# Optimization experiments

Measured on AMD Instinct MI355X. Metric: run time of the kernel, lower is better.

Reference implementation:

```python
import jax, jax.numpy as jnp
import numpy as np

TOPK = 2


def setup_inputs() -> dict:
    key = jax.random.key(0)
    k1, k2 = jax.random.split(key)
    B, N, D, E, C = 4, 2048, 2048, 8, 512
    token_inputs = jax.random.normal(k1, (B, N, D), dtype=jnp.float32)
    # bottleneck_in.weight.t() stacked over experts: [E, D, C]; scaled like a real init
    bottleneck_weights = jax.random.normal(k2, (E, D, C), dtype=jnp.float32) * 0.02
    return {
        "token_inputs": token_inputs,
        "bottleneck_weights": bottleneck_weights,
        "expert_capacity": 640,
    }


def _routing(router_probs, expert_capacity, topk):
    # router_probs: [B, N, E]
    B, N, E = router_probs.shape
    _, expert_indices = jax.lax.top_k(router_probs, topk)      # [B, N, topk]
    idx = jnp.transpose(expert_indices, (0, 2, 1)).reshape(B, topk * N)
    expert_mask = jax.nn.one_hot(idx, E, dtype=jnp.int32)       # [B, topk*N, E]
    token_priority = jnp.cumsum(expert_mask, axis=1) * expert_mask - 1
    token_priority = token_priority.reshape(B, topk, N, E)
    token_priority = jnp.transpose(token_priority, (0, 2, 1, 3))  # [B, N, topk, E]
    token_priority = jnp.max(token_priority, axis=2)              # [B, N, E]
    # one-hot over capacity; negative (-1) and >= capacity priorities map to all-zero rows
    cap_range = jnp.arange(expert_capacity, dtype=jnp.int32)
    dispatch = (token_priority[..., None] == cap_range).astype(jnp.float32)  # [B,N,E,C]
    combine = router_probs[..., None] * dispatch                            # [B,N,E,C]
    return dispatch, combine


def reference(token_inputs, bottleneck_weights, expert_capacity):
    # activation_cache: [B, N, E, Cb]
    activation_cache = jnp.einsum("bnd,edc->bnec", token_inputs, bottleneck_weights)
    router_logits = jnp.sqrt(jnp.sum(activation_cache * activation_cache, axis=-1))  # [B,N,E]
    router_probs = jax.nn.softmax(router_logits, axis=-1)
    dispatch, combine = _routing(router_probs, expert_capacity, TOPK)
    return jnp.stack([dispatch, combine], axis=0)  # [2, B, N, E, capacity]
```

## Files before the change

kernel.cpp:

```cpp
#include <hip/hip_runtime.h>
#include <math.h>

constexpr int Bb = 4, Nn = 2048, Dd = 2048, Ee = 8, Cbn = 512;
constexpr int Mm = Bb * Nn;

typedef _Float16 half8 __attribute__((ext_vector_type(8)));
typedef float floatx16 __attribute__((ext_vector_type(16)));

#define GLL16(g, l)                                                     \
  __builtin_amdgcn_global_load_lds(                                     \
      (const __attribute__((address_space(1))) void*)(g),               \
      (__attribute__((address_space(3))) void*)(l), 16, 0, 0)

#define MFMA_F16(a, b, c) __builtin_amdgcn_mfma_f32_32x32x16_f16(a, b, c, 0, 0, 0)


__global__ __launch_bounds__(256) void transpose_w(const float* __restrict__ W,
                                                   _Float16* __restrict__ WT) {
  const int kt = blockIdx.x;
  const int ct = blockIdx.y;
  const int e = blockIdx.z;
  __shared__ _Float16 thi[64][72];
  __shared__ _Float16 tlo[64][72];
  const int tx = threadIdx.x & 15, ty = threadIdx.x >> 4;
  const float* src = W + ((size_t)(e * 2048 + kt * 64)) * 512 + ct * 64;
#pragma unroll
  for (int p = 0; p < 4; ++p) {
    int kk = ty + p * 16;
    float4 v = *(const float4*)(src + (size_t)kk * 512 + tx * 4);
    _Float16 hh;
    hh = (_Float16)v.x; thi[tx * 4 + 0][kk] = hh; tlo[tx * 4 + 0][kk] = (_Float16)(v.x - (float)hh);
    hh = (_Float16)v.y; thi[tx * 4 + 1][kk] = hh; tlo[tx * 4 + 1][kk] = (_Float16)(v.y - (float)hh);
    hh = (_Float16)v.z; thi[tx * 4 + 2][kk] = hh; tlo[tx * 4 + 2][kk] = (_Float16)(v.z - (float)hh);
    hh = (_Float16)v.w; thi[tx * 4 + 3][kk] = hh; tlo[tx * 4 + 3][kk] = (_Float16)(v.w - (float)hh);
  }
  __syncthreads();
  const int ntile = e * 4 + (ct >> 1);
#pragma unroll
  for (int p = 0; p < 2; ++p) {
    int unit = threadIdx.x + p * 256;
    int ch = unit >> 6;
    int cc = unit & 63;
    int ktile = kt * 2 + (ch >> 2);
    int chunk = ch & 3;
    int row = (ct & 1) * 64 + cc;
    _Float16* dst = WT + ((size_t)(ntile * 64 + ktile)) * 8192 + chunk * 1024 + row * 8;
    *(half8*)dst = *(const half8*)(&thi[cc][ch * 8]);
    *(half8*)(dst + 4096) = *(const half8*)(&tlo[cc][ch * 8]);
  }
}

__global__ __launch_bounds__(256) void split_x(const float* __restrict__ X,
                                               _Float16* __restrict__ XT) {
  const int mt = blockIdx.x;
  const int kt = blockIdx.y;
  const int tid = threadIdx.x;
  _Float16* tb = XT + ((size_t)(mt * 64 + kt)) * 8192;
#pragma unroll
  for (int p = 0; p < 2; ++p) {
    const int u = tid + p * 256;
    const int chunk = u & 3;
    const int row = u >> 2;
    const float* src = X + ((size_t)(mt * 128 + row)) * 2048 + kt * 32 + chunk * 8;
    float4 a = *(const float4*)src;
    float4 b = *(const float4*)(src + 4);
    float f[8] = {a.x, a.y, a.z, a.w, b.x, b.y, b.z, b.w};
    half8 hi, lo;
#pragma unroll
    for (int j = 0; j < 8; ++j) {
      _Float16 hh = (_Float16)f[j];
      hi[j] = hh;
      lo[j] = (_Float16)(f[j] - (float)hh);
    }
    *(half8*)(tb + chunk * 1024 + row * 8) = hi;
    *(half8*)(tb + 4096 + chunk * 1024 + row * 8) = lo;
  }
}

__global__ __launch_bounds__(256) void gemm_mfma(const _Float16* __restrict__ XT,
                                                 const _Float16* __restrict__ WT,
                                                 float* __restrict__ partial) {
  const int bid = blockIdx.x;
  const int st = bid >> 8;
  const int stm = st & 3;
  const int stn = st >> 2;
  const int li = bid & 255;
  const int mtile = stm * 16 + (li >> 4);
  const int ntile = stn * 16 + (li & 15);

  const int tid = threadIdx.x;
  const int wave = tid >> 6, lane = tid & 63;
  const int wm = wave >> 1, wn = wave & 1;
  const int h = lane >> 5;

  __shared__ __align__(16) char lds[65536];

  const char* aSrc = (const char*)XT + (size_t)mtile * 64 * 16384 + wave * 4096 + lane * 16;
  const char* bSrc = (const char*)WT + (size_t)ntile * 64 * 16384 + wave * 4096 + lane * 16;

  const int rowA0 = wm * 64 + (lane & 31);
  const int rB0 = wn * 64 + (lane & 31);

  int aOff[2][2], bOff[2][2];
#pragma unroll
  for (int s = 0; s < 2; ++s)
#pragma unroll
    for (int hl = 0; hl < 2; ++hl) {
      aOff[s][hl] = hl * 8192 + (s * 2 + h) * 2048 + rowA0 * 16;
      bOff[s][hl] = 16384 + hl * 8192 + (s * 2 + h) * 2048 + rB0 * 16;
    }

  floatx16 acc00 = {}, acc01 = {}, acc10 = {}, acc11 = {};

#pragma unroll
  for (int q = 0; q < 4; ++q) {
    GLL16(aSrc + q * 1024, lds + wave * 4096 + q * 1024);
    GLL16(bSrc + q * 1024, lds + 16384 + wave * 4096 + q * 1024);
  }
  __syncthreads();

  for (int kt = 0; kt < 64; ++kt) {
    const int cur = kt & 1;
    if (kt < 63) {
      const char* a = aSrc + (size_t)(kt + 1) * 16384;
      const char* b = bSrc + (size_t)(kt + 1) * 16384;
      char* base = lds + (cur ^ 1) * 32768 + wave * 4096;
#pragma unroll
      for (int q = 0; q < 4; ++q) {
        GLL16(a + q * 1024, base + q * 1024);
        GLL16(b + q * 1024, base + 16384 + q * 1024);
      }
    }
    const char* L = lds + cur * 32768;
#pragma unroll
    for (int s = 0; s < 2; ++s) {
      half8 ah0 = *(const half8*)(L + aOff[s][0]);
      half8 ah1 = *(const half8*)(L + aOff[s][0] + 512);
      half8 al0 = *(const half8*)(L + aOff[s][1]);
      half8 al1 = *(const half8*)(L + aOff[s][1] + 512);
      half8 bh0 = *(const half8*)(L + bOff[s][0]);
      half8 bh1 = *(const half8*)(L + bOff[s][0] + 512);
      half8 bl0 = *(const half8*)(L + bOff[s][1]);
      half8 bl1 = *(const half8*)(L + bOff[s][1] + 512);
      acc00 = MFMA_F16(ah0, bh0, acc00);
      acc00 = MFMA_F16(ah0, bl0, acc00);
      acc00 = MFMA_F16(al0, bh0, acc00);
      acc01 = MFMA_F16(ah0, bh1, acc01);
      acc01 = MFMA_F16(ah0, bl1, acc01);
      acc01 = MFMA_F16(al0, bh1, acc01);
      acc10 = MFMA_F16(ah1, bh0, acc10);
      acc10 = MFMA_F16(ah1, bl0, acc10);
      acc10 = MFMA_F16(al1, bh0, acc10);
      acc11 = MFMA_F16(ah1, bh1, acc11);
      acc11 = MFMA_F16(ah1, bl1, acc11);
      acc11 = MFMA_F16(al1, bh1, acc11);
    }
    __syncthreads();
  }

  float myv = 0.f;
#pragma unroll
  for (int i = 0; i < 2; ++i) {
    const floatx16& c0 = i ? acc10 : acc00;
    const floatx16& c1 = i ? acc11 : acc01;
#pragma unroll
    for (int reg = 0; reg < 16; ++reg) {
      float v = c0[reg] * c0[reg] + c1[reg] * c1[reg];
#pragma unroll
      for (int m = 1; m <= 16; m <<= 1) v += __shfl_xor(v, m, 64);
      if ((lane & 31) == i * 16 + reg) myv = v;
    }
  }
  {
    const int i = (lane & 31) >> 4;
    const int reg = lane & 15;
    const int row = i * 32 + (reg & 3) + 8 * (reg >> 2) + 4 * h;
    const int token = mtile * 128 + wm * 64 + row;
    const int slice = ntile * 2 + wn;
    partial[(size_t)token * 64 + slice] = myv;
  }
}

__global__ void route_kernel(const float* __restrict__ partial,
                             int* __restrict__ idx1, int* __restrict__ idx2,
                             float* __restrict__ p1, float* __restrict__ p2) {
  int t = blockIdx.x * blockDim.x + threadIdx.x;
  if (t >= Mm) return;
  float l[Ee];
  float mx = -1e30f;
#pragma unroll
  for (int e = 0; e < Ee; ++e) {
    float s = 0.f;
#pragma unroll
    for (int u = 0; u < 8; ++u) s += partial[(size_t)t * 64 + e * 8 + u];
    l[e] = sqrtf(s);
    mx = fmaxf(mx, l[e]);
  }
  float p[Ee];
  float s = 0.f;
#pragma unroll
  for (int e = 0; e < Ee; ++e) {
    p[e] = expf(l[e] - mx);
    s += p[e];
  }
  float inv = 1.f / s;
  int i1 = 0;
  float b1 = l[0];
#pragma unroll
  for (int e = 1; e < Ee; ++e)
    if (l[e] > b1) { b1 = l[e]; i1 = e; }
  int i2 = -1;
  float b2 = -1e30f;
#pragma unroll
  for (int e = 0; e < Ee; ++e)
    if (e != i1 && l[e] > b2) { b2 = l[e]; i2 = e; }
  idx1[t] = i1;
  idx2[t] = i2;
  p1[t] = p[i1] * inv;
  p2[t] = p[i2] * inv;
}

__global__ void scan_kernel(const int* __restrict__ idx1,
                            const int* __restrict__ idx2,
                            int* __restrict__ prios) {
  const int b = blockIdx.x;
  const int tid = threadIdx.x;
  __shared__ int cnts[256][8];
  int cnt[8] = {0, 0, 0, 0, 0, 0, 0, 0};
  int eloc[16];
  const int base_p = tid * 16;
#pragma unroll
  for (int i = 0; i < 16; ++i) {
    int p = base_p + i;
    int k = p >> 11;
    int n = p & (Nn - 1);
    int e = (k == 0 ? idx1 : idx2)[b * Nn + n];
    eloc[i] = e;
    cnt[e]++;
  }
#pragma unroll
  for (int e = 0; e < 8; ++e) cnts[tid][e] = cnt[e];
  __syncthreads();
  if (tid < 8) {
    int run = 0;
    for (int i = 0; i < 256; ++i) {
      int v = cnts[i][tid];
      cnts[i][tid] = run;
      run += v;
    }
  }
  __syncthreads();
  int base[8];
#pragma unroll
  for (int e = 0; e < 8; ++e) base[e] = cnts[tid][e];
#pragma unroll
  for (int i = 0; i < 16; ++i) {
    int e = eloc[i];
    prios[b * 2 * Nn + base_p + i] = base[e]++;
  }
}

__global__ __launch_bounds__(256) void zscatter_kernel(const int* __restrict__ idx1,
                                                       const int* __restrict__ idx2,
                                                       const float* __restrict__ p1,
                                                       const float* __restrict__ p2,
                                                       const int* __restrict__ prios,
                                                       float* __restrict__ out, int cap) {
  const int t = blockIdx.x;
  const int ec = Ee * cap;
  float4* o1 = (float4*)(out + (size_t)t * ec);
  float4* o2 = (float4*)(out + (size_t)(Mm + t) * ec);
  const float4 z = make_float4(0.f, 0.f, 0.f, 0.f);
  const int n4 = ec / 4;
  for (int i = threadIdx.x; i < n4; i += 256) {
    o1[i] = z;
    o2[i] = z;
  }
  __syncthreads();
  if (threadIdx.x == 0) {
    const int b = t >> 11;
    const int n = t & (Nn - 1);
    int e = idx1[t];
    int p = prios[b * 2 * Nn + n];
    if (p < cap) {
      out[(size_t)t * ec + e * cap + p] = 1.f;
      out[(size_t)(Mm + t) * ec + e * cap + p] = p1[t];
    }
    e = idx2[t];
    p = prios[b * 2 * Nn + Nn + n];
    if (p < cap) {
      out[(size_t)t * ec + e * cap + p] = 1.f;
      out[(size_t)(Mm + t) * ec + e * cap + p] = p2[t];
    }
  }
}

extern "C" void kernel_launch(void* const* d_in, const int* in_sizes, int n_in,
                              void* d_out, int out_size, void* d_ws, size_t ws_size,
                              hipStream_t stream) {
  const float* X = (const float*)d_in[0];
  const float* W = (const float*)d_in[1];
  float* out = (float*)d_out;
  const int cap = out_size / (2 * Bb * Nn * Ee);

  char* ws = (char*)d_ws;
  _Float16* WT = (_Float16*)ws;
  float* partial = (float*)(ws + 33554432ull);
  int* idx1 = (int*)(ws + 35651584ull);
  int* idx2 = idx1 + Mm;
  float* p1 = (float*)(idx2 + Mm);
  float* p2 = p1 + Mm;
  int* prios = (int*)(p2 + Mm);

  _Float16* XT = (_Float16*)d_out;

  transpose_w<<<dim3(32, 8, 8), 256, 0, stream>>>(W, WT);
  split_x<<<dim3(64, 64), 256, 0, stream>>>(X, XT);
  gemm_mfma<<<2048, 256, 0, stream>>>(XT, WT, partial);
  route_kernel<<<Mm / 256, 256, 0, stream>>>(partial, idx1, idx2, p1, p2);
  scan_kernel<<<Bb, 256, 0, stream>>>(idx1, idx2, prios);
  zscatter_kernel<<<Mm, 256, 0, stream>>>(idx1, idx2, p1, p2, prios, out, cap);
}
```

Measured before the change: 777.3 us.

## Enlarge GEMM tiles to 256x256 with 4-stage LDS pipeline and K16 layout

```diff
diff --git a/kernel.cpp b/kernel.cpp
--- a/kernel.cpp
+++ b/kernel.cpp
@@ -35,33 +35,32 @@
     hh = (_Float16)v.w; thi[tx * 4 + 3][kk] = hh; tlo[tx * 4 + 3][kk] = (_Float16)(v.w - (float)hh);
   }
   __syncthreads();
-  const int ntile = e * 4 + (ct >> 1);
+  const int nt = e * 4 + (ct >> 1);
 #pragma unroll
   for (int p = 0; p < 2; ++p) {
     int unit = threadIdx.x + p * 256;
     int ch = unit >> 6;
     int cc = unit & 63;
-    int ktile = kt * 2 + (ch >> 2);
-    int chunk = ch & 3;
+    int kt16 = kt * 4 + (ch >> 1);
+    int chunk = ch & 1;
     int row = (ct & 1) * 64 + cc;
-    _Float16* dst = WT + ((size_t)(ntile * 64 + ktile)) * 8192 + chunk * 1024 + row * 8;
+    _Float16* dst = WT + ((size_t)(nt * 128 + kt16)) * 4096 + chunk * 1024 + row * 8;
     *(half8*)dst = *(const half8*)(&thi[cc][ch * 8]);
-    *(half8*)(dst + 4096) = *(const half8*)(&tlo[cc][ch * 8]);
+    *(half8*)(dst + 2048) = *(const half8*)(&tlo[cc][ch * 8]);
   }
 }
 
 __global__ __launch_bounds__(256) void split_x(const float* __restrict__ X,
                                                _Float16* __restrict__ XT) {
   const int mt = blockIdx.x;
-  const int kt = blockIdx.y;
+  const int kb = blockIdx.y;
   const int tid = threadIdx.x;
-  _Float16* tb = XT + ((size_t)(mt * 64 + kt)) * 8192;
 #pragma unroll
   for (int p = 0; p < 2; ++p) {
     const int u = tid + p * 256;
-    const int chunk = u & 3;
+    const int c4 = u & 3;
     const int row = u >> 2;
-    const float* src = X + ((size_t)(mt * 128 + row)) * 2048 + kt * 32 + chunk * 8;
+    const float* src = X + ((size_t)(mt * 128 + row)) * 2048 + kb * 32 + c4 * 8;
     float4 a = *(const float4*)src;
     float4 b = *(const float4*)(src + 4);
     float f[8] = {a.x, a.y, a.z, a.w, b.x, b.y, b.z, b.w};
@@ -72,112 +71,138 @@
       hi[j] = hh;
       lo[j] = (_Float16)(f[j] - (float)hh);
     }
-    *(half8*)(tb + chunk * 1024 + row * 8) = hi;
-    *(half8*)(tb + 4096 + chunk * 1024 + row * 8) = lo;
-  }
-}
-
-__global__ __launch_bounds__(256) void gemm_mfma(const _Float16* __restrict__ XT,
+    const int kt16 = kb * 2 + (c4 >> 1);
+    const int chunk = c4 & 1;
+    _Float16* dst = XT + ((size_t)(mt * 128 + kt16)) * 4096 + chunk * 1024 + row * 8;
+    *(half8*)dst = hi;
+    *(half8*)(dst + 2048) = lo;
+  }
+}
+
+__global__ __launch_bounds__(512) void gemm_mfma(const _Float16* __restrict__ XT,
                                                  const _Float16* __restrict__ WT,
                                                  float* __restrict__ partial) {
   const int bid = blockIdx.x;
-  const int st = bid >> 8;
-  const int stm = st & 3;
-  const int stn = st >> 2;
-  const int li = bid & 255;
-  const int mtile = stm * 16 + (li >> 4);
-  const int ntile = stn * 16 + (li & 15);
+  const int swz = (bid & 7) * 64 + (bid >> 3);
+  const int bM = swz >> 4;
+  const int bN = swz & 15;
 
   const int tid = threadIdx.x;
-  const int wave = tid >> 6, lane = tid & 63;
-  const int wm = wave >> 1, wn = wave & 1;
-  const int h = lane >> 5;
-
-  __shared__ __align__(16) char lds[65536];
-
-  const char* aSrc = (const char*)XT + (size_t)mtile * 64 * 16384 + wave * 4096 + lane * 16;
-  const char* bSrc = (const char*)WT + (size_t)ntile * 64 * 16384 + wave * 4096 + lane * 16;
-
-  const int rowA0 = wm * 64 + (lane & 31);
-  const int rB0 = wn * 64 + (lane & 31);
-
-  int aOff[2][2], bOff[2][2];
-#pragma unroll
-  for (int s = 0; s < 2; ++s)
-#pragma unroll
-    for (int hl = 0; hl < 2; ++hl) {
-      aOff[s][hl] = hl * 8192 + (s * 2 + h) * 2048 + rowA0 * 16;
-      bOff[s][hl] = 16384 + hl * 8192 + (s * 2 + h) * 2048 + rB0 * 16;
-    }
-
-  floatx16 acc00 = {}, acc01 = {}, acc10 = {}, acc11 = {};
-
-#pragma unroll
-  for (int q = 0; q < 4; ++q) {
-    GLL16(aSrc + q * 1024, lds + wave * 4096 + q * 1024);
-    GLL16(bSrc + q * 1024, lds + 16384 + wave * 4096 + q * 1024);
-  }
-  __syncthreads();
-
-  for (int kt = 0; kt < 64; ++kt) {
-    const int cur = kt & 1;
-    if (kt < 63) {
-      const char* a = aSrc + (size_t)(kt + 1) * 16384;
-      const char* b = bSrc + (size_t)(kt + 1) * 16384;
-      char* base = lds + (cur ^ 1) * 32768 + wave * 4096;
-#pragma unroll
-      for (int q = 0; q < 4; ++q) {
-        GLL16(a + q * 1024, base + q * 1024);
-        GLL16(b + q * 1024, base + 16384 + q * 1024);
+  const int w = tid >> 6, l = tid & 63;
+  const int wm = w >> 2, wn = w & 3;
+  const int h = l >> 5, l31 = l & 31;
+
+  __shared__ __align__(16) char lds[131072];
+
+  const char* XTb = (const char*)XT;
+  const char* WTb = (const char*)WT;
+  const char* srcA[2];
+  const char* srcB[2];
+  int ldsAo[2], ldsBo[2];
+#pragma unroll
+  for (int q = 0; q < 2; ++q) {
+    const int i3 = q * 4 + (w >> 1);
+    srcA[q] = XTb + ((size_t)((bM * 2 + (i3 >> 2)) * 128)) * 8192 +
+              (i3 & 3) * 2048 + (w & 1) * 1024 + l * 16;
+    srcB[q] = WTb + ((size_t)((bN * 2 + (i3 >> 2)) * 128)) * 8192 +
+              (i3 & 3) * 2048 + (w & 1) * 1024 + l * 16;
+    ldsAo[q] = q * 8192 + w * 1024;
+    ldsBo[q] = 16384 + q * 8192 + w * 1024;
+  }
+
+  int aoff[4][2], boff[2][2];
+#pragma unroll
+  for (int mf = 0; mf < 4; ++mf)
+#pragma unroll
+    for (int hl = 0; hl < 2; ++hl)
+      aoff[mf][hl] = wm * 8192 + hl * 4096 + h * 2048 + (mf * 32 + l31) * 16;
+#pragma unroll
+  for (int nf = 0; nf < 2; ++nf)
+#pragma unroll
+    for (int hl = 0; hl < 2; ++hl)
+      boff[nf][hl] = 16384 + (wn >> 1) * 8192 + hl * 4096 + h * 2048 +
+                     ((wn & 1) * 64 + nf * 32 + l31) * 16;
+
+  floatx16 acc[4][2] = {};
+
+  auto stage = [&](int t) {
+    const size_t ko = (size_t)t * 8192;
+    char* base = lds + (t & 3) * 32768;
+#pragma unroll
+    for (int q = 0; q < 2; ++q) {
+      GLL16(srcA[q] + ko, base + ldsAo[q]);
+      GLL16(srcB[q] + ko, base + ldsBo[q]);
+    }
+  };
+  auto compute = [&](int t) {
+    const char* Lb = lds + (t & 3) * 32768;
+    half8 ah[4], al[4], bh[2], bl[2];
+#pragma unroll
+    for (int mf = 0; mf < 4; ++mf) {
+      ah[mf] = *(const half8*)(Lb + aoff[mf][0]);
+      al[mf] = *(const half8*)(Lb + aoff[mf][1]);
+    }
+#pragma unroll
+    for (int nf = 0; nf < 2; ++nf) {
+      bh[nf] = *(const half8*)(Lb + boff[nf][0]);
+      bl[nf] = *(const half8*)(Lb + boff[nf][1]);
+    }
+    __builtin_amdgcn_s_setprio(1);
+#pragma unroll
+    for (int mf = 0; mf < 4; ++mf)
+#pragma unroll
+      for (int nf = 0; nf < 2; ++nf) {
+        acc[mf][nf] = MFMA_F16(ah[mf], bh[nf], acc[mf][nf]);
+        acc[mf][nf] = MFMA_F16(ah[mf], bl[nf], acc[mf][nf]);
+        acc[mf][nf] = MFMA_F16(al[mf], bh[nf], acc[mf][nf]);
       }
-    }
-    const char* L = lds + cur * 32768;
-#pragma unroll
-    for (int s = 0; s < 2; ++s) {
-      half8 ah0 = *(const half8*)(L + aOff[s][0]);
-      half8 ah1 = *(const half8*)(L + aOff[s][0] + 512);
-      half8 al0 = *(const half8*)(L + aOff[s][1]);
-      half8 al1 = *(const half8*)(L + aOff[s][1] + 512);
-      half8 bh0 = *(const half8*)(L + bOff[s][0]);
-      half8 bh1 = *(const half8*)(L + bOff[s][0] + 512);
-      half8 bl0 = *(const half8*)(L + bOff[s][1]);
-      half8 bl1 = *(const half8*)(L + bOff[s][1] + 512);
-      acc00 = MFMA_F16(ah0, bh0, acc00);
-      acc00 = MFMA_F16(ah0, bl0, acc00);
-      acc00 = MFMA_F16(al0, bh0, acc00);
-      acc01 = MFMA_F16(ah0, bh1, acc01);
-      acc01 = MFMA_F16(ah0, bl1, acc01);
-      acc01 = MFMA_F16(al0, bh1, acc01);
-      acc10 = MFMA_F16(ah1, bh0, acc10);
-      acc10 = MFMA_F16(ah1, bl0, acc10);
-      acc10 = MFMA_F16(al1, bh0, acc10);
-      acc11 = MFMA_F16(ah1, bh1, acc11);
-      acc11 = MFMA_F16(ah1, bl1, acc11);
-      acc11 = MFMA_F16(al1, bh1, acc11);
-    }
-    __syncthreads();
-  }
-
-  float myv = 0.f;
-#pragma unroll
-  for (int i = 0; i < 2; ++i) {
-    const floatx16& c0 = i ? acc10 : acc00;
-    const floatx16& c1 = i ? acc11 : acc01;
-#pragma unroll
-    for (int reg = 0; reg < 16; ++reg) {
-      float v = c0[reg] * c0[reg] + c1[reg] * c1[reg];
-#pragma unroll
-      for (int m = 1; m <= 16; m <<= 1) v += __shfl_xor(v, m, 64);
-      if ((lane & 31) == i * 16 + reg) myv = v;
-    }
+    __builtin_amdgcn_s_setprio(0);
+  };
+
+  stage(0);
+  stage(1);
+  stage(2);
+  asm volatile("s_waitcnt vmcnt(8)" ::: "memory");
+  __builtin_amdgcn_s_barrier();
+
+  for (int kt = 0; kt < 125; ++kt) {
+    stage(kt + 3);
+    compute(kt);
+    asm volatile("s_waitcnt vmcnt(8)" ::: "memory");
+    __builtin_amdgcn_s_barrier();
+  }
+  asm volatile("s_waitcnt vmcnt(0)" ::: "memory");
+  __builtin_amdgcn_s_barrier();
+  compute(125);
+  compute(126);
+  compute(127);
+
+  const int slice = bN * 4 + wn;
+  float out0 = 0.f, out1 = 0.f;
+#pragma unroll
+  for (int j = 0; j < 2; ++j) {
+    float mv = 0.f;
+#pragma unroll
+    for (int ii = 0; ii < 2; ++ii) {
+      const floatx16& c0 = acc[j * 2 + ii][0];
+      const floatx16& c1 = acc[j * 2 + ii][1];
+#pragma unroll
+      for (int reg = 0; reg < 16; ++reg) {
+        float v = c0[reg] * c0[reg] + c1[reg] * c1[reg];
+#pragma unroll
+        for (int m = 1; m <= 16; m <<= 1) v += __shfl_xor(v, m, 64);
+        if (l31 == ii * 16 + reg) mv = v;
+      }
+    }
+    if (j == 0) out0 = mv; else out1 = mv;
   }
   {
-    const int i = (lane & 31) >> 4;
-    const int reg = lane & 15;
-    const int row = i * 32 + (reg & 3) + 8 * (reg >> 2) + 4 * h;
-    const int token = mtile * 128 + wm * 64 + row;
-    const int slice = ntile * 2 + wn;
-    partial[(size_t)token * 64 + slice] = myv;
+    const int reg = l & 15;
+    const int ii = l31 >> 4;
+    const int rowin = (reg & 3) + 8 * (reg >> 2) + 4 * h;
+    const int tok = bM * 256 + wm * 128 + ii * 32 + rowin;
+    partial[(size_t)tok * 64 + slice] = out0;
+    partial[(size_t)(tok + 64) * 64 + slice] = out1;
   }
 }
 
@@ -316,7 +341,7 @@
 
   transpose_w<<<dim3(32, 8, 8), 256, 0, stream>>>(W, WT);
   split_x<<<dim3(64, 64), 256, 0, stream>>>(X, XT);
-  gemm_mfma<<<2048, 256, 0, stream>>>(XT, WT, partial);
+  gemm_mfma<<<512, 512, 0, stream>>>(XT, WT, partial);
   route_kernel<<<Mm / 256, 256, 0, stream>>>(partial, idx1, idx2, p1, p2);
   scan_kernel<<<Bb, 256, 0, stream>>>(idx1, idx2, prios);
   zscatter_kernel<<<Mm, 256, 0, stream>>>(idx1, idx2, p1, p2, prios, out, cap);
```

New measurement: 757.5 us. 1.03x faster.
